# Optimization experiments

Hardware: AMD Instinct MI355X
Metric: run time of the kernel (lower is better)

The kernel has to match this reference:

```python
import jax, jax.numpy as jnp
import numpy as np

HEADS, DIM_HEAD = 16, 64
MAX_FREQ = 256.0

def axial_freqs(H, W):
    # rotary_embedding_torch, freqs_for='pixel': base freqs = linspace(1, max_freq/2, dim//2)*pi
    # with rotary dim = DIM_HEAD//2 per axis, so DIM_HEAD//4 base frequencies per axis.
    nf = DIM_HEAD // 4
    base = jnp.linspace(1.0, MAX_FREQ / 2.0, nf) * jnp.pi
    def per_axis(n):
        pos = jnp.linspace(-1.0, 1.0, n)              # pixel positions in [-1, 1]
        fr = pos[:, None] * base[None, :]             # (n, DIM_HEAD//4)
        return jnp.repeat(fr, 2, axis=-1)             # (n, DIM_HEAD//2), interleaved repeat
    fh = jnp.broadcast_to(per_axis(H)[:, None, :], (H, W, DIM_HEAD // 2))
    fw = jnp.broadcast_to(per_axis(W)[None, :, :], (H, W, DIM_HEAD // 2))
    return jnp.concatenate([fh, fw], axis=-1)         # (H, W, DIM_HEAD)

def rotate_half(x):
    # interleaved-pair rotation: (x0,x1,x2,x3,...) -> (-x1,x0,-x3,x2,...)
    x2 = x.reshape(x.shape[:-1] + (-1, 2))
    a, b = x2[..., 0], x2[..., 1]
    return jnp.stack([-b, a], axis=-1).reshape(x.shape)

def apply_rot(freqs, t):
    return t * jnp.cos(freqs) + rotate_half(t) * jnp.sin(freqs)

def setup_inputs() -> dict:
    key = jax.random.key(0)
    ks = jax.random.split(key, 6)
    B, T, H, W, dim = 1, 2, 16, 16, 1024
    inner = HEADS * DIM_HEAD
    S, K = H * W, 144
    x = jax.random.normal(ks[0], (B, T, H, W, dim), jnp.float32)
    w_qkv = jax.random.normal(ks[1], (3 * inner, dim), jnp.float32) * (dim ** -0.5)
    w_out = jax.random.normal(ks[2], (dim, inner), jnp.float32) * (inner ** -0.5)
    b_out = jnp.zeros((dim,), jnp.float32)
    out_not_top_k = jax.random.normal(ks[3], (B * T, HEADS, S, DIM_HEAD), jnp.float32) * 0.02
    top_k_indices = jax.random.randint(ks[4], (B * T, HEADS, S, K), 0, S, jnp.int32)
    return {"x": x, "w_qkv": w_qkv, "w_out": w_out, "b_out": b_out,
            "out_not_top_k": out_not_top_k, "top_k_indices": top_k_indices}

def reference(x, w_qkv, w_out, b_out, out_not_top_k, top_k_indices):
    B, T, H, W, dim = x.shape
    inner = HEADS * DIM_HEAD
    S = H * W
    # qkv projection (torch Linear: y = x @ W^T)
    qkv = jnp.einsum('bthwc,oc->bthwo', x, w_qkv)
    q, k, v = jnp.split(qkv, 3, axis=-1)

    def to_grid(t):
        t = t.reshape(B * T, H, W, HEADS, DIM_HEAD)
        return jnp.transpose(t, (0, 3, 1, 2, 4))       # (BT, h, H, W, d)
    q, k, v = map(to_grid, (q, k, v))

    freqs = axial_freqs(H, W)                          # (H, W, d), broadcasts over (BT, h)
    q = apply_rot(freqs, q)
    k = apply_rot(freqs, k)

    q = q.reshape(B * T, HEADS, S, DIM_HEAD)
    k = k.reshape(B * T, HEADS, S, DIM_HEAD)
    v = v.reshape(B * T, HEADS, S, DIM_HEAD)

    scale = DIM_HEAD ** -0.5
    idx = top_k_indices[..., None]                      # (BT, h, S, K, 1)
    # per-query gather of top-k keys/values: out[b,h,s,k,:] = k[b,h,idx[b,h,s,k],:]
    k_g = jnp.take_along_axis(k[:, :, None, :, :], idx, axis=3)  # (BT, h, S, K, d)
    v_g = jnp.take_along_axis(v[:, :, None, :, :], idx, axis=3)

    scores = jnp.einsum('bhsd,bhskd->bhsk', q, k_g) * scale
    probs = jax.nn.softmax(scores, axis=-1)
    out_top = jnp.einsum('bhsk,bhskd->bhsd', probs, v_g)

    out = out_top + out_not_top_k                       # (BT, h, S, d)
    out = jnp.transpose(out.reshape(B * T, HEADS, H, W, DIM_HEAD), (0, 2, 3, 1, 4))
    out = out.reshape(B, T, H, W, inner)
    return jnp.einsum('bthwi,oi->bthwo', out, w_out) + b_out
```

## Files before the change

kernel.cpp:

```cpp
#include <hip/hip_runtime.h>
#include <hip/hip_bf16.h>
#include <math.h>

#define BTN   2
#define NH    16
#define SEQ   256
#define DH    64
#define DIMF  1024
#define KTOP  144
#define QT    16
#define PI_F  3.14159265358979323846f

typedef _Float16 half8 __attribute__((ext_vector_type(8)));
typedef _Float16 half4v __attribute__((ext_vector_type(4)));
typedef float f32x4 __attribute__((ext_vector_type(4)));

#define GLDS(src, dst) __builtin_amdgcn_global_load_lds( \
        (const __attribute__((address_space(1))) void*)(src), \
        (__attribute__((address_space(3))) void*)(dst), 16, 0, 0)

#define N0Q (524288 / 4)
#define N1Q (3145728 / 4)
#define N2Q (1048576 / 4)
__global__ __launch_bounds__(256)
void cvt3_kernel(const float* __restrict__ a, const float* __restrict__ b,
                 const float* __restrict__ c,
                 _Float16* __restrict__ da, _Float16* __restrict__ db,
                 _Float16* __restrict__ dc)
{
    int q = blockIdx.x * 256 + threadIdx.x;
    const float* s; _Float16* d; int off;
    if (q < N0Q)            { s = a; d = da; off = q; }
    else if (q < N0Q + N1Q) { s = b; d = db; off = q - N0Q; }
    else                    { s = c; d = dc; off = q - (N0Q + N1Q); }
    const float4 v = *(const float4*)(s + (size_t)off * 4);
    half4v h;
    h[0] = (_Float16)v.x; h[1] = (_Float16)v.y;
    h[2] = (_Float16)v.z; h[3] = (_Float16)v.w;
    *(half4v*)(d + (size_t)off * 4) = h;
}

template <int MODE, int Kd>
__global__ __launch_bounds__(256)
void gemm_f16_kernel(const _Float16* __restrict__ A, const _Float16* __restrict__ B,
                     int N,
                     _Float16* __restrict__ qb, _Float16* __restrict__ kb,
                     _Float16* __restrict__ vb,
                     const float* __restrict__ bias, float* __restrict__ out)
{
    __shared__ __align__(16) _Float16 As[64 * 64];
    __shared__ __align__(16) _Float16 Bs[64 * 64];

    const int tid  = threadIdx.x;
    const int wave = tid >> 6;
    const int lane = tid & 63;
    const int row0 = blockIdx.y * 64;
    const int col0 = blockIdx.x * 64;
    const int wr = (wave >> 1) * 32;
    const int wc = (wave & 1) * 32;
    const int rl = lane >> 3;
    const int cl = lane & 7;

    f32x4 acc[2][2] = {};

    for (int kt = 0; kt < Kd; kt += 64) {
        __syncthreads();
#pragma unroll
        for (int h = 0; h < 2; ++h) {
            const int rbase = wave * 16 + h * 8;
            const int rA = rbase + rl;
            const _Float16* srcA = A + (size_t)(row0 + rA) * Kd + kt + ((cl ^ (rA & 7)) * 8);
            const _Float16* srcB = B + (size_t)(col0 + rA) * Kd + kt + ((cl ^ (rA & 7)) * 8);
            GLDS(srcA, As + rbase * 64);
            GLDS(srcB, Bs + rbase * 64);
        }
        __syncthreads();

#pragma unroll
        for (int kh = 0; kh < 2; ++kh) {
            half8 a[2], b[2];
            const int g = kh * 4 + (lane >> 4);
#pragma unroll
            for (int i = 0; i < 2; ++i) {
                const int ra = wr + i * 16 + (lane & 15);
                const int rb = wc + i * 16 + (lane & 15);
                a[i] = *(const half8*)(As + ra * 64 + ((g ^ (ra & 7)) * 8));
                b[i] = *(const half8*)(Bs + rb * 64 + ((g ^ (rb & 7)) * 8));
            }
#pragma unroll
            for (int i = 0; i < 2; ++i)
#pragma unroll
                for (int j = 0; j < 2; ++j)
                    acc[i][j] = __builtin_amdgcn_mfma_f32_16x16x32_f16(a[i], b[j], acc[i][j], 0, 0, 0);
        }
    }

    if (MODE == 0) {
#pragma unroll
        for (int i = 0; i < 2; ++i) {
#pragma unroll
            for (int reg = 0; reg < 4; ++reg) {
                const int r  = row0 + wr + i * 16 + (lane >> 4) * 4 + reg;
                const int bt = r >> 8;
                const int s  = r & 255;
                const int hh = s >> 4;
                const int ww = s & 15;
#pragma unroll
                for (int j = 0; j < 2; ++j) {
                    const float v     = acc[i][j][reg];
                    const float other = __shfl_xor(v, 1);
                    const int n    = col0 + wc + j * 16 + (lane & 15);
                    const int sec  = n >> 10;
                    const int oi   = n & 1023;
                    const int head = oi >> 6;
                    const int d    = oi & 63;
                    if (sec == 2) {
                        vb[(((size_t)(bt * NH + head)) * DH + d) * SEQ + s] = (_Float16)v;
                    } else {
                        const int de  = d & ~1;
                        const int j2  = (de < 32) ? (de >> 1) : ((de - 32) >> 1);
                        const float pos = (de < 32) ? (-1.f + hh * (2.f / 15.f))
                                                    : (-1.f + ww * (2.f / 15.f));
                        const float f  = pos * (PI_F * (1.f + j2 * (127.f / 15.f)));
                        const float cf = __cosf(f), sf = __sinf(f);
                        const float res = (d & 1) ? (v * cf + other * sf)
                                                  : (v * cf - other * sf);
                        _Float16* dp = (sec == 0) ? qb : kb;
                        dp[(((size_t)(bt * NH + head)) * SEQ + s) * DH + d] = (_Float16)res;
                    }
                }
            }
        }
    } else {
#pragma unroll
        for (int i = 0; i < 2; ++i)
#pragma unroll
            for (int reg = 0; reg < 4; ++reg) {
                const int r = row0 + wr + i * 16 + (lane >> 4) * 4 + reg;
#pragma unroll
                for (int j = 0; j < 2; ++j) {
                    const int n = col0 + wc + j * 16 + (lane & 15);
                    out[(size_t)r * N + n] = acc[i][j][reg] + bias[n];
                }
            }
    }
}

__global__ __launch_bounds__(256)
void attn_reg16_kernel(const _Float16* __restrict__ qh, const _Float16* __restrict__ kh,
                       const _Float16* __restrict__ vt, const int* __restrict__ topk,
                       const float* __restrict__ ontk, _Float16* __restrict__ attnh)
{
    __shared__ __align__(16) float Ps[QT * 256];

    const int tid  = threadIdx.x;
    const int w    = tid >> 6;
    const int lane = tid & 63;
    const int bid  = blockIdx.x;
    const int bt   = bid >> 8;
    const int head = (bid >> 4) & 15;
    const int s0   = (bid & 15) * QT;
    const int bh   = bt * NH + head;

    half8 aq[2], bk[2][4];
#pragma unroll
    for (int kk = 0; kk < 2; ++kk) {
        const int c8 = (kk * 4 + (lane >> 4)) * 8;
        aq[kk] = *(const half8*)(qh + ((size_t)bh * SEQ + s0 + (lane & 15)) * DH + c8);
#pragma unroll
        for (int j = 0; j < 4; ++j)
            bk[kk][j] = *(const half8*)(kh + ((size_t)bh * SEQ + w * 64 + j * 16 + (lane & 15)) * DH + c8);
    }
    int ki0[4], ki1[4], ki2[4];
#pragma unroll
    for (int qq = 0; qq < 4; ++qq) {
        const int* idxp = topk + ((size_t)bh * SEQ + s0 + w * 4 + qq) * KTOP;
        ki0[qq] = idxp[lane];
        ki1[qq] = idxp[lane + 64];
        ki2[qq] = idxp[(lane < 16) ? (lane + 128) : lane];
    }
    half8 bv[8];
    {
        const _Float16* vrow = vt + ((size_t)bh * DH + w * 16 + (lane & 15)) * SEQ
                                  + (lane >> 4) * 8;
#pragma unroll
        for (int ks = 0; ks < 8; ++ks)
            bv[ks] = *(const half8*)(vrow + ks * 32);
    }
    float on[4];
#pragma unroll
    for (int reg = 0; reg < 4; ++reg) {
        const int row = (lane >> 4) * 4 + reg;
        on[reg] = ontk[((size_t)bh * SEQ + s0 + row) * DH + w * 16 + (lane & 15)];
    }

    f32x4 acc[4] = {};
#pragma unroll
    for (int kk = 0; kk < 2; ++kk)
#pragma unroll
        for (int j = 0; j < 4; ++j)
            acc[j] = __builtin_amdgcn_mfma_f32_16x16x32_f16(aq[kk], bk[kk][j], acc[j], 0, 0, 0);
#pragma unroll
    for (int j = 0; j < 4; ++j)
#pragma unroll
        for (int reg = 0; reg < 4; ++reg) {
            const int row = (lane >> 4) * 4 + reg;
            const int col = w * 64 + j * 16 + (lane & 15);
            Ps[row * 256 + (col ^ ((row & 7) << 2))] = acc[j][reg];
        }
    __syncthreads();

#pragma unroll
    for (int qq = 0; qq < 4; ++qq) {
        const int q  = w * 4 + qq;
        const int sw = (q & 7) << 2;
        float* prow  = Ps + q * 256;
        const float sv0 = prow[ki0[qq] ^ sw] * 0.125f;
        const float sv1 = prow[ki1[qq] ^ sw] * 0.125f;
        const float sv2 = (lane < 16) ? prow[ki2[qq] ^ sw] * 0.125f : -1e30f;
        float m = fmaxf(fmaxf(sv0, sv1), sv2);
#pragma unroll
        for (int off = 32; off; off >>= 1) m = fmaxf(m, __shfl_xor(m, off));
        const float e0 = __expf(sv0 - m);
        const float e1 = __expf(sv1 - m);
        const float e2 = (lane < 16) ? __expf(sv2 - m) : 0.f;
        float z = e0 + e1 + e2;
#pragma unroll
        for (int off = 32; off; off >>= 1) z += __shfl_xor(z, off);
        const float inv = 1.f / z;
#pragma unroll
        for (int c2 = 0; c2 < 4; ++c2) prow[lane + c2 * 64] = 0.f;
        atomicAdd(&prow[ki0[qq] ^ sw], e0 * inv);
        atomicAdd(&prow[ki1[qq] ^ sw], e1 * inv);
        if (lane < 16) atomicAdd(&prow[ki2[qq] ^ sw], e2 * inv);
    }
    __syncthreads();

    f32x4 oacc = {};
#pragma unroll
    for (int ks = 0; ks < 8; ++ks) {
        const int ra = lane & 15;
        const int b0 = ks * 32 + (lane >> 4) * 8;
        const int sw = (ra & 7) << 2;
        const float4 p0 = *(const float4*)(Ps + ra * 256 + (b0 ^ sw));
        const float4 p1 = *(const float4*)(Ps + ra * 256 + ((b0 + 4) ^ sw));
        half8 af;
        af[0] = (_Float16)p0.x; af[1] = (_Float16)p0.y;
        af[2] = (_Float16)p0.z; af[3] = (_Float16)p0.w;
        af[4] = (_Float16)p1.x; af[5] = (_Float16)p1.y;
        af[6] = (_Float16)p1.z; af[7] = (_Float16)p1.w;
        oacc = __builtin_amdgcn_mfma_f32_16x16x32_f16(af, bv[ks], oacc, 0, 0, 0);
    }
#pragma unroll
    for (int reg = 0; reg < 4; ++reg) {
        const int row = (lane >> 4) * 4 + reg;
        const int d   = w * 16 + (lane & 15);
        const int s   = s0 + row;
        attnh[((size_t)(bt * SEQ + s)) * DIMF + head * DH + d] = (_Float16)(oacc[reg] + on[reg]);
    }
}

extern "C" void kernel_launch(void* const* d_in, const int* in_sizes, int n_in,
                              void* d_out, int out_size, void* d_ws, size_t ws_size,
                              hipStream_t stream) {
    const float* x     = (const float*)d_in[0];
    const float* w_qkv = (const float*)d_in[1];
    const float* w_out = (const float*)d_in[2];
    const float* b_out = (const float*)d_in[3];
    const float* ontk  = (const float*)d_in[4];
    const int*   topk  = (const int*)d_in[5];
    float* out = (float*)d_out;

    const size_t QE = (size_t)BTN * NH * SEQ * DH;

    _Float16* xh    = (_Float16*)d_ws;
    _Float16* wqh   = xh + 524288;
    _Float16* woh   = wqh + 3145728;
    _Float16* attnh = woh + 1048576;
    _Float16* qhb   = attnh + QE;
    _Float16* khb   = qhb + QE;
    _Float16* vtb   = khb + QE;

    cvt3_kernel<<<(N0Q + N1Q + N2Q) / 256, 256, 0, stream>>>(x, w_qkv, w_out, xh, wqh, woh);

    gemm_f16_kernel<0, DIMF><<<dim3(3072 / 64, 512 / 64), 256, 0, stream>>>(
        xh, wqh, 3072, qhb, khb, vtb, nullptr, nullptr);

    attn_reg16_kernel<<<BTN * NH * (SEQ / QT), 256, 0, stream>>>(
        qhb, khb, vtb, topk, ontk, attnh);

    gemm_f16_kernel<1, DIMF><<<dim3(1024 / 64, 512 / 64), 256, 0, stream>>>(
        attnh, woh, 1024, nullptr, nullptr, nullptr, b_out, out);
}
```

Before: 49.36 us.

## Fuse fp32-to-fp16 conversion into GEMM tile loads, drop conversion kernel

Removes the standalone conversion kernel and has both projection GEMMs load fp32 x and weight tiles directly into LDS via global_load_lds, converting to fp16 while reading fragments for MFMA. This eliminates one launch and the write and re-read of fp16 copies of the inputs and weights. In exchange, LDS usage per block doubles for the fp32 tiles, and each GEMM reads twice the bytes per tile, with conversion work repeated across blocks sharing a tile.

```diff
diff --git a/kernel.cpp b/kernel.cpp
--- a/kernel.cpp
+++ b/kernel.cpp
@@ -12,45 +12,25 @@
 #define PI_F  3.14159265358979323846f
 
 typedef _Float16 half8 __attribute__((ext_vector_type(8)));
-typedef _Float16 half4v __attribute__((ext_vector_type(4)));
 typedef float f32x4 __attribute__((ext_vector_type(4)));
 
 #define GLDS(src, dst) __builtin_amdgcn_global_load_lds( \
         (const __attribute__((address_space(1))) void*)(src), \
         (__attribute__((address_space(3))) void*)(dst), 16, 0, 0)
 
-#define N0Q (524288 / 4)
-#define N1Q (3145728 / 4)
-#define N2Q (1048576 / 4)
+template <int MODE>
 __global__ __launch_bounds__(256)
-void cvt3_kernel(const float* __restrict__ a, const float* __restrict__ b,
-                 const float* __restrict__ c,
-                 _Float16* __restrict__ da, _Float16* __restrict__ db,
-                 _Float16* __restrict__ dc)
+void gemm_mixed_kernel(const float* __restrict__ A32, const _Float16* __restrict__ A16,
+                       const float* __restrict__ B32, int N,
+                       _Float16* __restrict__ qb, _Float16* __restrict__ kb,
+                       _Float16* __restrict__ vb,
+                       const float* __restrict__ bias, float* __restrict__ out)
 {
-    int q = blockIdx.x * 256 + threadIdx.x;
-    const float* s; _Float16* d; int off;
-    if (q < N0Q)            { s = a; d = da; off = q; }
-    else if (q < N0Q + N1Q) { s = b; d = db; off = q - N0Q; }
-    else                    { s = c; d = dc; off = q - (N0Q + N1Q); }
-    const float4 v = *(const float4*)(s + (size_t)off * 4);
-    half4v h;
-    h[0] = (_Float16)v.x; h[1] = (_Float16)v.y;
-    h[2] = (_Float16)v.z; h[3] = (_Float16)v.w;
-    *(half4v*)(d + (size_t)off * 4) = h;
-}
-
-template <int MODE, int Kd>
-__global__ __launch_bounds__(256)
-void gemm_f16_kernel(const _Float16* __restrict__ A, const _Float16* __restrict__ B,
-                     int N,
-                     _Float16* __restrict__ qb, _Float16* __restrict__ kb,
-                     _Float16* __restrict__ vb,
-                     const float* __restrict__ bias, float* __restrict__ out)
-{
-    __shared__ __align__(16) _Float16 As[64 * 64];
-    __shared__ __align__(16) _Float16 Bs[64 * 64];
-
+    __shared__ __align__(16) float Bs32[64 * 64];
+    __shared__ __align__(16) float As32[(MODE == 0) ? 64 * 64 : 32 * 64];
+    _Float16* As16 = (_Float16*)As32;
+
+    const int Kd   = DIMF;
     const int tid  = threadIdx.x;
     const int wave = tid >> 6;
     const int lane = tid & 63;
@@ -58,21 +38,39 @@
     const int col0 = blockIdx.x * 64;
     const int wr = (wave >> 1) * 32;
     const int wc = (wave & 1) * 32;
-    const int rl = lane >> 3;
-    const int cl = lane & 7;
+
+    const int rl4 = lane >> 4;
+    const int cl16 = lane & 15;
+    const int rl8 = lane >> 3;
+    const int cl8 = lane & 7;
 
     f32x4 acc[2][2] = {};
 
     for (int kt = 0; kt < Kd; kt += 64) {
         __syncthreads();
-#pragma unroll
-        for (int h = 0; h < 2; ++h) {
-            const int rbase = wave * 16 + h * 8;
-            const int rA = rbase + rl;
-            const _Float16* srcA = A + (size_t)(row0 + rA) * Kd + kt + ((cl ^ (rA & 7)) * 8);
-            const _Float16* srcB = B + (size_t)(col0 + rA) * Kd + kt + ((cl ^ (rA & 7)) * 8);
-            GLDS(srcA, As + rbase * 64);
-            GLDS(srcB, Bs + rbase * 64);
+        if (MODE == 0) {
+#pragma unroll
+            for (int h = 0; h < 4; ++h) {
+                const int r = wave * 16 + h * 4 + rl4;
+                const int co = ((((cl16 >> 1) ^ (r & 7)) << 3) + ((cl16 & 1) << 2));
+                GLDS(A32 + (size_t)(row0 + r) * Kd + kt + co,
+                     As32 + (wave * 16 + h * 4) * 64);
+            }
+        } else {
+#pragma unroll
+            for (int h = 0; h < 2; ++h) {
+                const int rbase = wave * 16 + h * 8;
+                const int rA = rbase + rl8;
+                GLDS(A16 + (size_t)(row0 + rA) * Kd + kt + ((cl8 ^ (rA & 7)) * 8),
+                     As16 + rbase * 64);
+            }
+        }
+#pragma unroll
+        for (int h = 0; h < 4; ++h) {
+            const int r = wave * 16 + h * 4 + rl4;
+            const int co = ((((cl16 >> 1) ^ (r & 7)) << 3) + ((cl16 & 1) << 2));
+            GLDS(B32 + (size_t)(col0 + r) * Kd + kt + co,
+                 Bs32 + (wave * 16 + h * 4) * 64);
         }
         __syncthreads();
 
@@ -83,9 +81,27 @@
 #pragma unroll
             for (int i = 0; i < 2; ++i) {
                 const int ra = wr + i * 16 + (lane & 15);
+                if (MODE == 0) {
+                    const float* p = As32 + ra * 64 + ((g ^ (ra & 7)) * 8);
+                    const f32x4 lo = *(const f32x4*)p;
+                    const f32x4 hi = *(const f32x4*)(p + 4);
+#pragma unroll
+                    for (int t = 0; t < 4; ++t) {
+                        a[i][t]     = (_Float16)lo[t];
+                        a[i][t + 4] = (_Float16)hi[t];
+                    }
+                } else {
+                    a[i] = *(const half8*)(As16 + ra * 64 + ((g ^ (ra & 7)) * 8));
+                }
                 const int rb = wc + i * 16 + (lane & 15);
-                a[i] = *(const half8*)(As + ra * 64 + ((g ^ (ra & 7)) * 8));
-                b[i] = *(const half8*)(Bs + rb * 64 + ((g ^ (rb & 7)) * 8));
+                const float* q = Bs32 + rb * 64 + ((g ^ (rb & 7)) * 8);
+                const f32x4 lo = *(const f32x4*)q;
+                const f32x4 hi = *(const f32x4*)(q + 4);
+#pragma unroll
+                for (int t = 0; t < 4; ++t) {
+                    b[i][t]     = (_Float16)lo[t];
+                    b[i][t + 4] = (_Float16)hi[t];
+                }
             }
 #pragma unroll
             for (int i = 0; i < 2; ++i)
@@ -273,22 +289,17 @@
 
     const size_t QE = (size_t)BTN * NH * SEQ * DH;
 
-    _Float16* xh    = (_Float16*)d_ws;
-    _Float16* wqh   = xh + 524288;
-    _Float16* woh   = wqh + 3145728;
-    _Float16* attnh = woh + 1048576;
-    _Float16* qhb   = attnh + QE;
+    _Float16* attnh = (_Float16*)d_ws;
+    _Float16* qhb   = attnh + (size_t)512 * 1024;
     _Float16* khb   = qhb + QE;
     _Float16* vtb   = khb + QE;
 
-    cvt3_kernel<<<(N0Q + N1Q + N2Q) / 256, 256, 0, stream>>>(x, w_qkv, w_out, xh, wqh, woh);
-
-    gemm_f16_kernel<0, DIMF><<<dim3(3072 / 64, 512 / 64), 256, 0, stream>>>(
-        xh, wqh, 3072, qhb, khb, vtb, nullptr, nullptr);
+    gemm_mixed_kernel<0><<<dim3(3072 / 64, 512 / 64), 256, 0, stream>>>(
+        x, nullptr, w_qkv, 3072, qhb, khb, vtb, nullptr, nullptr);
 
     attn_reg16_kernel<<<BTN * NH * (SEQ / QT), 256, 0, stream>>>(
         qhb, khb, vtb, topk, ontk, attnh);
 
-    gemm_f16_kernel<1, DIMF><<<dim3(1024 / 64, 512 / 64), 256, 0, stream>>>(
-        attnh, woh, 1024, nullptr, nullptr, nullptr, b_out, out);
+    gemm_mixed_kernel<1><<<dim3(1024 / 64, 512 / 64), 256, 0, stream>>>(
+        nullptr, attnh, w_out, 1024, nullptr, nullptr, nullptr, b_out, out);
 }
```

Measured after the change: 52.51 us. +6.4%, slower.
